# Optimization experiments

Hardware: AMD Instinct MI355X
Metric: run time of the kernel (lower is better)

## Reference

```python
import jax, jax.numpy as jnp
import numpy as np

N = 500_000   # nodes
D = 256       # feature dim
S = 20_000    # segments (pooled outputs)


def setup_inputs() -> dict:
    key = jax.random.key(0)
    ks = jax.random.split(key, 6)
    x = jax.random.normal(ks[0], (N, D), dtype=jnp.float32)
    # weights must be strictly positive (raised to a learned power)
    weights = jax.random.uniform(ks[1], (N, 1), dtype=jnp.float32) + 0.01
    Wg = jax.random.normal(ks[2], (D, 1), dtype=jnp.float32) / np.sqrt(D)
    bg = jnp.zeros((1,), dtype=jnp.float32)
    Wm = jax.random.normal(ks[3], (D, D), dtype=jnp.float32) / np.sqrt(D)
    bm = jnp.zeros((D,), dtype=jnp.float32)
    p = jax.random.normal(ks[4], (1,), dtype=jnp.float32)
    index = jnp.sort(jax.random.randint(ks[5], (N,), 0, S, dtype=jnp.int32))
    return {"x": x, "weights": weights, "Wg": Wg, "bg": bg, "Wm": Wm,
            "bm": bm, "p": p, "index": index, "num_segments": S}


def reference(x, weights, Wg, bg, Wm, bm, p, index, num_segments):
    # gate_nn: per-node attention logit [N, 1]
    gate = x @ Wg + bg
    # segment-wise max subtraction for numerical stability
    seg_max = jax.ops.segment_max(gate, index, num_segments=num_segments)
    gate = gate - seg_max[index]
    # weighted exponential: weights ** pow * exp(gate)
    gate = (weights ** p) * jnp.exp(gate)
    # segment-wise normalization (softmax denominator)
    denom = jax.ops.segment_sum(gate, index, num_segments=num_segments)
    gate = gate / (denom[index] + 1e-10)
    # message_nn: per-node messages [N, D]
    msg = x @ Wm + bm
    # attention-weighted segment sum -> [S, D]
    return jax.ops.segment_sum(gate * msg, index, num_segments=num_segments)
```

## Files before the change

### kernel.cpp

```cpp
#include <hip/hip_runtime.h>

#define DDIM 256
#define CHUNK 512
#define WCHUNK 128
#define TM 64
#define TN 64
#define TK 16

__global__ __launch_bounds__(256) void k_gate(
    const float* __restrict__ x, const float* __restrict__ Wg,
    const float* __restrict__ bg, const int* __restrict__ index,
    float* __restrict__ gate, unsigned* __restrict__ segmax, int N)
{
    const int lane = threadIdx.x & 63;
    const int wave = threadIdx.x >> 6;
    const float4 wg = ((const float4*)Wg)[lane];
    const float b = bg[0];
    int row0 = (blockIdx.x * 4 + wave) * 8;
    for (int r = 0; r < 8; ++r) {
        int row = row0 + r;
        if (row >= N) return;
        float4 xv = ((const float4*)x)[(size_t)row * (DDIM/4) + lane];
        float d = xv.x*wg.x + xv.y*wg.y + xv.z*wg.z + xv.w*wg.w;
        #pragma unroll
        for (int m = 32; m >= 1; m >>= 1) d += __shfl_xor(d, m, 64);
        if (lane == 0) {
            float g = d + b;
            gate[row] = g;
            unsigned bits = __float_as_uint(g);
            unsigned enc = (bits & 0x80000000u) ? ~bits : (bits | 0x80000000u);
            atomicMax(&segmax[index[row]], enc);
        }
    }
}

__global__ __launch_bounds__(256) void k_weight(
    const float* __restrict__ weights, const float* __restrict__ p_,
    const int* __restrict__ index, const unsigned* __restrict__ segmax,
    float* __restrict__ gate, float* __restrict__ denom, int N)
{
    int i = blockIdx.x * 256 + threadIdx.x;
    if (i >= N) return;
    float p = p_[0];
    int s = index[i];
    unsigned u = segmax[s];
    unsigned bits = (u & 0x80000000u) ? (u & 0x7FFFFFFFu) : ~u;
    float m = __uint_as_float(bits);
    float w = powf(weights[i], p) * expf(gate[i] - m);
    gate[i] = w;
    atomicAdd(&denom[s], w);
}

__global__ __launch_bounds__(256) void k_pool(
    const float* __restrict__ x, const int* __restrict__ index,
    const float* __restrict__ gate, const float* __restrict__ denom,
    float* __restrict__ pooled, int N)
{
    __shared__ int   s_seg[CHUNK];
    __shared__ float s_g[CHUNK];
    const int n0 = blockIdx.x * CHUNK;
    for (int jj = threadIdx.x; jj < CHUNK; jj += 256) {
        int i = n0 + jj;
        if (i < N) {
            int s = index[i];
            s_seg[jj] = s;
            s_g[jj] = gate[i] / (denom[s] + 1e-10f);
        } else {
            s_seg[jj] = -1;
        }
    }
    __syncthreads();
    const int lane = threadIdx.x & 63;
    const int wave = threadIdx.x >> 6;
    const int j0 = wave * WCHUNK;
    const float4* x4 = (const float4*)x;
    float4 acc = make_float4(0.f, 0.f, 0.f, 0.f);
    int prev = -1;
    for (int j = j0; j < j0 + WCHUNK; ++j) {
        int i = n0 + j;
        if (i >= N) break;
        int s = s_seg[j];
        if (s != prev) {
            if (prev >= 0) {
                float* pp = &pooled[(size_t)prev * DDIM + lane * 4];
                atomicAdd(pp + 0, acc.x); atomicAdd(pp + 1, acc.y);
                atomicAdd(pp + 2, acc.z); atomicAdd(pp + 3, acc.w);
            }
            acc = make_float4(0.f, 0.f, 0.f, 0.f);
            prev = s;
        }
        float g = s_g[j];
        float4 xv = x4[(size_t)i * (DDIM/4) + lane];
        acc.x += g * xv.x; acc.y += g * xv.y;
        acc.z += g * xv.z; acc.w += g * xv.w;
    }
    if (prev >= 0) {
        float* pp = &pooled[(size_t)prev * DDIM + lane * 4];
        atomicAdd(pp + 0, acc.x); atomicAdd(pp + 1, acc.y);
        atomicAdd(pp + 2, acc.z); atomicAdd(pp + 3, acc.w);
    }
}

__global__ __launch_bounds__(256) void k_gemm(
    const float* __restrict__ pooled, const float* __restrict__ Wm,
    const float* __restrict__ bm, const float* __restrict__ denom,
    float* __restrict__ out, int S)
{
    __shared__ float At[TK][TM + 4];
    __shared__ float Bs[TK][TN];
    const int tx = threadIdx.x & 15;
    const int ty = threadIdx.x >> 4;
    const int r0 = blockIdx.x * TM;
    const int c0 = blockIdx.y * TN;
    float acc[4][4] = {};

    for (int k0 = 0; k0 < DDIM; k0 += TK) {
        {
            int t = threadIdx.x;
            int r = t >> 2;
            int kq = (t & 3) * 4;
            float4 a = make_float4(0.f, 0.f, 0.f, 0.f);
            if (r0 + r < S)
                a = *(const float4*)&pooled[(size_t)(r0 + r) * DDIM + k0 + kq];
            At[kq + 0][r] = a.x; At[kq + 1][r] = a.y;
            At[kq + 2][r] = a.z; At[kq + 3][r] = a.w;
        }
        {
            int t = threadIdx.x;
            int k = t >> 4;
            int cq = (t & 15) * 4;
            float4 bv = *(const float4*)&Wm[(size_t)(k0 + k) * DDIM + c0 + cq];
            *(float4*)&Bs[k][cq] = bv;
        }
        __syncthreads();
        #pragma unroll
        for (int k = 0; k < TK; ++k) {
            const float4 av = *(const float4*)&At[k][ty * 4];
            const float4 bv = *(const float4*)&Bs[k][tx * 4];
            float a4[4] = {av.x, av.y, av.z, av.w};
            float b4[4] = {bv.x, bv.y, bv.z, bv.w};
            #pragma unroll
            for (int i = 0; i < 4; ++i)
                #pragma unroll
                for (int j = 0; j < 4; ++j)
                    acc[i][j] += a4[i] * b4[j];
        }
        __syncthreads();
    }

    const float4 bmv = *(const float4*)&bm[c0 + tx * 4];
    #pragma unroll
    for (int i = 0; i < 4; ++i) {
        int row = r0 + ty * 4 + i;
        if (row >= S) continue;
        float dn = denom[row];
        float gs = dn / (dn + 1e-10f);
        float4 o;
        o.x = acc[i][0] + gs * bmv.x;
        o.y = acc[i][1] + gs * bmv.y;
        o.z = acc[i][2] + gs * bmv.z;
        o.w = acc[i][3] + gs * bmv.w;
        *(float4*)&out[(size_t)row * DDIM + c0 + tx * 4] = o;
    }
}

extern "C" void kernel_launch(void* const* d_in, const int* in_sizes, int n_in,
                              void* d_out, int out_size, void* d_ws, size_t ws_size,
                              hipStream_t stream) {
    const float* x       = (const float*)d_in[0];
    const float* weights = (const float*)d_in[1];
    const float* Wg      = (const float*)d_in[2];
    const float* bg      = (const float*)d_in[3];
    const float* Wm      = (const float*)d_in[4];
    const float* bm      = (const float*)d_in[5];
    const float* p       = (const float*)d_in[6];
    const int*   index   = (const int*)d_in[7];

    const int N = in_sizes[1];
    const int D = in_sizes[2];
    const int S = out_size / D;
    float* out = (float*)d_out;

    float*    gate   = (float*)d_ws;
    unsigned* segmax = (unsigned*)(gate + N);
    float*    denom  = (float*)(segmax + S);
    float*    pooled = denom + S;

    hipMemsetAsync(segmax, 0, (size_t)S * sizeof(unsigned), stream);
    hipMemsetAsync(denom,  0, (size_t)S * sizeof(float), stream);
    hipMemsetAsync(pooled, 0, (size_t)S * D * sizeof(float), stream);

    k_gate  <<<(N + 31) / 32,        256, 0, stream>>>(x, Wg, bg, index, gate, segmax, N);
    k_weight<<<(N + 255) / 256,      256, 0, stream>>>(weights, p, index, segmax, gate, denom, N);
    k_pool  <<<(N + CHUNK-1)/CHUNK,  256, 0, stream>>>(x, index, gate, denom, pooled, N);

    dim3 g5((S + TM - 1) / TM, D / TN);
    k_gemm  <<<g5, 256, 0, stream>>>(pooled, Wm, bm, denom, out, S);
}
```

Before: 899.8 us.

## Fuse gate, weighting and pooling into one pass and defer softmax normalization

Replaces the separate gate, weight and pool kernels with one fused kernel that reads each row of x once. That single read computes the gate dot product with a wave reduction, forms pow(w,p)*exp(gate), and accumulates both the weighted features and the per-segment denominator. Normalization by the denominator moves into the epilogue of the final GEMM, and the GEMM K tile is doubled. The segment-max subtraction is dropped, which saves a full pass over x but removes overflow protection for large gate logits.

```diff
diff --git a/kernel.cpp b/kernel.cpp
--- a/kernel.cpp
+++ b/kernel.cpp
@@ -1,81 +1,45 @@
 #include <hip/hip_runtime.h>
+#include <math.h>
 
 #define DDIM 256
 #define CHUNK 512
 #define WCHUNK 128
 #define TM 64
 #define TN 64
-#define TK 16
+#define TK 32
 
-__global__ __launch_bounds__(256) void k_gate(
-    const float* __restrict__ x, const float* __restrict__ Wg,
-    const float* __restrict__ bg, const int* __restrict__ index,
-    float* __restrict__ gate, unsigned* __restrict__ segmax, int N)
-{
-    const int lane = threadIdx.x & 63;
-    const int wave = threadIdx.x >> 6;
-    const float4 wg = ((const float4*)Wg)[lane];
-    const float b = bg[0];
-    int row0 = (blockIdx.x * 4 + wave) * 8;
-    for (int r = 0; r < 8; ++r) {
-        int row = row0 + r;
-        if (row >= N) return;
-        float4 xv = ((const float4*)x)[(size_t)row * (DDIM/4) + lane];
-        float d = xv.x*wg.x + xv.y*wg.y + xv.z*wg.z + xv.w*wg.w;
-        #pragma unroll
-        for (int m = 32; m >= 1; m >>= 1) d += __shfl_xor(d, m, 64);
-        if (lane == 0) {
-            float g = d + b;
-            gate[row] = g;
-            unsigned bits = __float_as_uint(g);
-            unsigned enc = (bits & 0x80000000u) ? ~bits : (bits | 0x80000000u);
-            atomicMax(&segmax[index[row]], enc);
-        }
-    }
-}
-
-__global__ __launch_bounds__(256) void k_weight(
-    const float* __restrict__ weights, const float* __restrict__ p_,
-    const int* __restrict__ index, const unsigned* __restrict__ segmax,
-    float* __restrict__ gate, float* __restrict__ denom, int N)
-{
-    int i = blockIdx.x * 256 + threadIdx.x;
-    if (i >= N) return;
-    float p = p_[0];
-    int s = index[i];
-    unsigned u = segmax[s];
-    unsigned bits = (u & 0x80000000u) ? (u & 0x7FFFFFFFu) : ~u;
-    float m = __uint_as_float(bits);
-    float w = powf(weights[i], p) * expf(gate[i] - m);
-    gate[i] = w;
-    atomicAdd(&denom[s], w);
-}
-
-__global__ __launch_bounds__(256) void k_pool(
-    const float* __restrict__ x, const int* __restrict__ index,
-    const float* __restrict__ gate, const float* __restrict__ denom,
-    float* __restrict__ pooled, int N)
+__global__ __launch_bounds__(256) void k_fused(
+    const float* __restrict__ x, const float* __restrict__ weights,
+    const float* __restrict__ Wg, const float* __restrict__ bg,
+    const float* __restrict__ p_, const int* __restrict__ index,
+    float* __restrict__ pooled, float* __restrict__ denom, int N)
 {
     __shared__ int   s_seg[CHUNK];
-    __shared__ float s_g[CHUNK];
+    __shared__ float s_wp[CHUNK];
     const int n0 = blockIdx.x * CHUNK;
+    const float p = p_[0];
     for (int jj = threadIdx.x; jj < CHUNK; jj += 256) {
         int i = n0 + jj;
         if (i < N) {
-            int s = index[i];
-            s_seg[jj] = s;
-            s_g[jj] = gate[i] / (denom[s] + 1e-10f);
+            s_seg[jj] = index[i];
+            s_wp[jj]  = powf(weights[i], p);
         } else {
             s_seg[jj] = -1;
         }
     }
     __syncthreads();
+
     const int lane = threadIdx.x & 63;
     const int wave = threadIdx.x >> 6;
+    const float4 wg = ((const float4*)Wg)[lane];
+    const float b = bg[0];
     const int j0 = wave * WCHUNK;
     const float4* x4 = (const float4*)x;
+
     float4 acc = make_float4(0.f, 0.f, 0.f, 0.f);
+    float wsum = 0.f;
     int prev = -1;
+
     for (int j = j0; j < j0 + WCHUNK; ++j) {
         int i = n0 + j;
         if (i >= N) break;
@@ -85,19 +49,26 @@
                 float* pp = &pooled[(size_t)prev * DDIM + lane * 4];
                 atomicAdd(pp + 0, acc.x); atomicAdd(pp + 1, acc.y);
                 atomicAdd(pp + 2, acc.z); atomicAdd(pp + 3, acc.w);
+                if (lane == 0) atomicAdd(&denom[prev], wsum);
             }
             acc = make_float4(0.f, 0.f, 0.f, 0.f);
+            wsum = 0.f;
             prev = s;
         }
-        float g = s_g[j];
         float4 xv = x4[(size_t)i * (DDIM/4) + lane];
-        acc.x += g * xv.x; acc.y += g * xv.y;
-        acc.z += g * xv.z; acc.w += g * xv.w;
+        float d = xv.x*wg.x + xv.y*wg.y + xv.z*wg.z + xv.w*wg.w;
+        #pragma unroll
+        for (int m = 32; m >= 1; m >>= 1) d += __shfl_xor(d, m, 64);
+        float w = s_wp[j] * __expf(d + b);
+        acc.x += w * xv.x; acc.y += w * xv.y;
+        acc.z += w * xv.z; acc.w += w * xv.w;
+        wsum += w;
     }
     if (prev >= 0) {
         float* pp = &pooled[(size_t)prev * DDIM + lane * 4];
         atomicAdd(pp + 0, acc.x); atomicAdd(pp + 1, acc.y);
         atomicAdd(pp + 2, acc.z); atomicAdd(pp + 3, acc.w);
+        if (lane == 0) atomicAdd(&denom[prev], wsum);
     }
 }
 
@@ -115,22 +86,24 @@
     float acc[4][4] = {};
 
     for (int k0 = 0; k0 < DDIM; k0 += TK) {
-        {
-            int t = threadIdx.x;
-            int r = t >> 2;
-            int kq = (t & 3) * 4;
-            float4 a = make_float4(0.f, 0.f, 0.f, 0.f);
-            if (r0 + r < S)
-                a = *(const float4*)&pooled[(size_t)(r0 + r) * DDIM + k0 + kq];
-            At[kq + 0][r] = a.x; At[kq + 1][r] = a.y;
-            At[kq + 2][r] = a.z; At[kq + 3][r] = a.w;
-        }
-        {
-            int t = threadIdx.x;
-            int k = t >> 4;
-            int cq = (t & 15) * 4;
-            float4 bv = *(const float4*)&Wm[(size_t)(k0 + k) * DDIM + c0 + cq];
-            *(float4*)&Bs[k][cq] = bv;
+        #pragma unroll
+        for (int it = 0; it < 2; ++it) {
+            int idx = threadIdx.x + it * 256;
+            {
+                int r  = idx >> 3;
+                int kq = (idx & 7) * 4;
+                float4 a = make_float4(0.f, 0.f, 0.f, 0.f);
+                if (r0 + r < S)
+                    a = *(const float4*)&pooled[(size_t)(r0 + r) * DDIM + k0 + kq];
+                At[kq + 0][r] = a.x; At[kq + 1][r] = a.y;
+                At[kq + 2][r] = a.z; At[kq + 3][r] = a.w;
+            }
+            {
+                int k  = idx >> 4;
+                int cq = (idx & 15) * 4;
+                *(float4*)&Bs[k][cq] =
+                    *(const float4*)&Wm[(size_t)(k0 + k) * DDIM + c0 + cq];
+            }
         }
         __syncthreads();
         #pragma unroll
@@ -154,12 +127,13 @@
         int row = r0 + ty * 4 + i;
         if (row >= S) continue;
         float dn = denom[row];
-        float gs = dn / (dn + 1e-10f);
+        float scale = 1.f / (dn + 1e-10f);
+        float gs = dn * scale;
         float4 o;
-        o.x = acc[i][0] + gs * bmv.x;
-        o.y = acc[i][1] + gs * bmv.y;
-        o.z = acc[i][2] + gs * bmv.z;
-        o.w = acc[i][3] + gs * bmv.w;
+        o.x = acc[i][0] * scale + gs * bmv.x;
+        o.y = acc[i][1] * scale + gs * bmv.y;
+        o.z = acc[i][2] * scale + gs * bmv.z;
+        o.w = acc[i][3] * scale + gs * bmv.w;
         *(float4*)&out[(size_t)row * DDIM + c0 + tx * 4] = o;
     }
 }
@@ -181,19 +155,15 @@
     const int S = out_size / D;
     float* out = (float*)d_out;
 
-    float*    gate   = (float*)d_ws;
-    unsigned* segmax = (unsigned*)(gate + N);
-    float*    denom  = (float*)(segmax + S);
-    float*    pooled = denom + S;
+    float* denom  = (float*)d_ws;
+    float* pooled = denom + S;
 
-    hipMemsetAsync(segmax, 0, (size_t)S * sizeof(unsigned), stream);
     hipMemsetAsync(denom,  0, (size_t)S * sizeof(float), stream);
     hipMemsetAsync(pooled, 0, (size_t)S * D * sizeof(float), stream);
 
-    k_gate  <<<(N + 31) / 32,        256, 0, stream>>>(x, Wg, bg, index, gate, segmax, N);
-    k_weight<<<(N + 255) / 256,      256, 0, stream>>>(weights, p, index, segmax, gate, denom, N);
-    k_pool  <<<(N + CHUNK-1)/CHUNK,  256, 0, stream>>>(x, index, gate, denom, pooled, N);
+    k_fused<<<(N + CHUNK - 1) / CHUNK, 256, 0, stream>>>(
+        x, weights, Wg, bg, p, index, pooled, denom, N);
 
-    dim3 g5((S + TM - 1) / TM, D / TN);
-    k_gemm  <<<g5, 256, 0, stream>>>(pooled, Wm, bm, denom, out, S);
+    dim3 g2((S + TM - 1) / TM, D / TN);
+    k_gemm<<<g2, 256, 0, stream>>>(pooled, Wm, bm, denom, out, S);
 }
```

Measured after the change: 749.9 us. 1.2x faster.
